# Kernel optimization log

Hardware: AMD Instinct MI355X
Metric: run time of the kernel (lower is better)

## Reference

```python
import jax, jax.numpy as jnp
import numpy as np

H = 1024  # n_hidden
T = 8192  # sequence length


def setup_inputs() -> dict:
    key = jax.random.key(0)
    ks = jax.random.split(key, 11)
    s = 1.0 / np.sqrt(H)  # torch LSTMCell/Linear default init scale
    u = lambda k, shape: jax.random.uniform(k, shape, jnp.float32, -s, s)
    return {
        "sequence": jax.random.normal(ks[0], (1, T), jnp.float32),
        # lstm1: input size 1 -> hidden H
        "w_ih1": u(ks[1], (4 * H, 1)),
        "w_hh1": u(ks[2], (4 * H, H)),
        "b_ih1": u(ks[3], (4 * H,)),
        "b_hh1": u(ks[4], (4 * H,)),
        # lstm2: hidden H -> hidden H
        "w_ih2": u(ks[5], (4 * H, H)),
        "w_hh2": u(ks[6], (4 * H, H)),
        "b_ih2": u(ks[7], (4 * H,)),
        "b_hh2": u(ks[8], (4 * H,)),
        # final linear: H -> 1
        "w_lin": u(ks[9], (1, H)),
        "b_lin": u(ks[10], (1,)),
    }


def _lstm_cell(x, h, c, w_ih, w_hh, b_ih, b_hh):
    # x: [1, in], h/c: [1, H]. PyTorch LSTMCell gate order: i, f, g, o
    gates = x @ w_ih.T + h @ w_hh.T + (b_ih + b_hh)  # [1, 4H]
    i, f, g, o = jnp.split(gates, 4, axis=-1)
    i = jax.nn.sigmoid(i)
    f = jax.nn.sigmoid(f)
    g = jnp.tanh(g)
    o = jax.nn.sigmoid(o)
    c_new = f * c + i * g
    h_new = o * jnp.tanh(c_new)
    return h_new, c_new


def reference(sequence, w_ih1, w_hh1, b_ih1, b_hh1,
              w_ih2, w_hh2, b_ih2, b_hh2, w_lin, b_lin):
    n = sequence.shape[0]  # 1
    z = jnp.zeros((n, w_hh1.shape[1]), jnp.float32)
    init = (z, z, z, z)  # h1, c1, h2, c2
    xs = sequence.T[:, :, None]  # [T, 1, 1] timesteps

    def step(carry, x_t):
        h1, c1, h2, c2 = carry
        h1, c1 = _lstm_cell(x_t, h1, c1, w_ih1, w_hh1, b_ih1, b_hh1)
        h2, c2 = _lstm_cell(h1, h2, c2, w_ih2, w_hh2, b_ih2, b_hh2)
        out = h2 @ w_lin.T + b_lin  # [1, 1]
        return (h1, c1, h2, c2), out

    _, outputs = jax.lax.scan(step, init, xs)
    return outputs  # [T, 1, 1] — stacked version of the original list of [1,1] outputs
```

## Files before the change

kernel.cpp:

```cpp
#include <hip/hip_runtime.h>

#define HID   1024
#define SEQT  8192
#define NBLK  256
#define TPB   512

#define WS_BYTES 32768

typedef float v16f __attribute__((ext_vector_type(16)));
typedef unsigned long long u64;

__device__ __forceinline__ float sig_(float x) { return 1.0f / (1.0f + expf(-x)); }

__device__ __forceinline__ u64 ldp(const u64* p) {
    return __hip_atomic_load(p, __ATOMIC_RELAXED, __HIP_MEMORY_SCOPE_AGENT);
}
__device__ __forceinline__ void stp(u64* p, u64 v) {
    __hip_atomic_store(p, v, __ATOMIC_RELAXED, __HIP_MEMORY_SCOPE_AGENT);
}

extern "C" __global__ void __launch_bounds__(TPB, 2)
lstm_hyb(const float* __restrict__ seq,
         const float* __restrict__ w_ih1, const float* __restrict__ w_hh1,
         const float* __restrict__ b_ih1, const float* __restrict__ b_hh1,
         const float* __restrict__ w_ih2, const float* __restrict__ w_hh2,
         const float* __restrict__ b_ih2, const float* __restrict__ b_hh2,
         const float* __restrict__ w_lin, const float* __restrict__ b_lin,
         float* __restrict__ out, u64* ws)
{
    __shared__ float h1s[HID];
    __shared__ float h2s[HID];
    __shared__ float seqs[SEQT];

    const int  lane = threadIdx.x & 63;
    const int  widx = threadIdx.x >> 6;
    const bool isL1 = (widx < 4);
    const int  r    = blockIdx.x * 4 + (widx & 3);

    u64* h1t = ws;
    u64* h2t = ws + 2048;

    for (int i = threadIdx.x; i < SEQT; i += TPB) seqs[i] = seq[i];

    const float* bA  = isL1 ? w_hh1 : w_ih2;
    const float* bB  = isL1 ? w_hh1 : w_hh2;
    const float* bbi = isL1 ? b_ih1 : b_ih2;
    const float* bbh = isL1 ? b_hh1 : b_hh2;
    const float  zmask = isL1 ? 0.f : 1.f;
    const float  xsel  = isL1 ? 1.f : 0.f;

    v16f A0, A1, A2, A3, B0, B1, B2, B3;
    {
        const size_t ro = (size_t)r * HID + lane;
        const float *a0 = bA + ro, *a1 = bA + (size_t)HID * HID + ro,
                    *a2 = bA + 2 * (size_t)HID * HID + ro, *a3 = bA + 3 * (size_t)HID * HID + ro;
        const float *b0 = bB + ro, *b1 = bB + (size_t)HID * HID + ro,
                    *b2 = bB + 2 * (size_t)HID * HID + ro, *b3 = bB + 3 * (size_t)HID * HID + ro;
#pragma unroll
        for (int k = 0; k < 16; ++k) {
            A0[k] = a0[64 * k]; A1[k] = a1[64 * k]; A2[k] = a2[64 * k]; A3[k] = a3[64 * k];
            B0[k] = b0[64 * k]; B1[k] = b1[64 * k]; B2[k] = b2[64 * k]; B3[k] = b3[64 * k];
        }
    }
    const float wx0 = w_ih1[0 * HID + r], wx1 = w_ih1[1 * HID + r],
                wx2 = w_ih1[2 * HID + r], wx3 = w_ih1[3 * HID + r];
    const float bb0 = bbi[0 * HID + r] + bbh[0 * HID + r];
    const float bb1 = bbi[1 * HID + r] + bbh[1 * HID + r];
    const float bb2 = bbi[2 * HID + r] + bbh[2 * HID + r];
    const float bb3 = bbi[3 * HID + r] + bbh[3 * HID + r];

    const bool carrier = (blockIdx.x == 0 && widx == 7);
    v16f WL; float blin = 0.f;
#pragma unroll
    for (int k = 0; k < 16; ++k) WL[k] = 0.f;
    if (carrier) {
#pragma unroll
        for (int k = 0; k < 16; ++k) WL[k] = w_lin[lane + 64 * k];
        blin = b_lin[0];
    }

    u64* pub = isL1 ? h1t : h2t;
    float c = 0.f;

    for (int t = 0; t <= SEQT + 1; ++t) {
        if (widx == 0 && t <= SEQT) {
            const u64* p = h1t + ((t + 1) & 1) * HID + lane;
            int guard = 0;
            for (;;) {
                int mn = 0x7fffffff;
#pragma unroll
                for (int k = 0; k < 16; ++k) {
                    u64 q = ldp(p + 64 * k);
                    h1s[lane + 64 * k] = __uint_as_float((unsigned)q);
                    mn = min(mn, (int)(q >> 32));
                }
                if (__all(mn >= t)) break;
                if (++guard > (1 << 14)) break;
            }
        }
        if (widx == 4) {
            const u64* p = h2t + (t & 1) * HID + lane;
            const int thr = t - 1;
            int guard = 0;
            for (;;) {
                int mn = 0x7fffffff;
#pragma unroll
                for (int k = 0; k < 16; ++k) {
                    u64 q = ldp(p + 64 * k);
                    h2s[lane + 64 * k] = __uint_as_float((unsigned)q);
                    mn = min(mn, (int)(q >> 32));
                }
                if (__all(mn >= thr)) break;
                if (++guard > (1 << 14)) break;
            }
        }
        __syncthreads();

        const bool act = isL1 ? (t < SEQT) : (t >= 1 && t <= SEQT);
        if (act) {
            v16f v1, v2;
#pragma unroll
            for (int k = 0; k < 16; ++k) {
                v1[k] = h1s[lane + 64 * k];
                v2[k] = h2s[lane + 64 * k] * zmask;
            }
            float a0 = 0.f, a1 = 0.f, a2 = 0.f, a3 = 0.f;
#pragma unroll
            for (int k = 0; k < 16; ++k) {
                a0 = fmaf(A0[k], v1[k], a0);
                a1 = fmaf(A1[k], v1[k], a1);
                a2 = fmaf(A2[k], v1[k], a2);
                a3 = fmaf(A3[k], v1[k], a3);
            }
#pragma unroll
            for (int k = 0; k < 16; ++k) {
                a0 = fmaf(B0[k], v2[k], a0);
                a1 = fmaf(B1[k], v2[k], a1);
                a2 = fmaf(B2[k], v2[k], a2);
                a3 = fmaf(B3[k], v2[k], a3);
            }
#pragma unroll
            for (int s = 32; s; s >>= 1) {
                a0 += __shfl_xor(a0, s);
                a1 += __shfl_xor(a1, s);
                a2 += __shfl_xor(a2, s);
                a3 += __shfl_xor(a3, s);
            }
            const float xg = xsel * ((t < SEQT) ? seqs[t] : 0.f);
            float i_ = sig_(a0 + xg * wx0 + bb0);
            float f_ = sig_(a1 + xg * wx1 + bb1);
            float g_ = tanhf(a2 + xg * wx2 + bb2);
            float o_ = sig_(a3 + xg * wx3 + bb3);
            c = f_ * c + i_ * g_;
            float h = o_ * tanhf(c);
            if (lane == 0) {
                const int ps = isL1 ? t : (t - 1);
                stp(pub + (ps & 1) * HID + r,
                    ((u64)(unsigned)(ps + 1) << 32) | (u64)__float_as_uint(h));
            }
        }

        if (carrier && t >= 2) {
            float ov = 0.f;
#pragma unroll
            for (int k = 0; k < 16; ++k) ov = fmaf(WL[k], h2s[lane + 64 * k], ov);
#pragma unroll
            for (int s = 32; s; s >>= 1) ov += __shfl_xor(ov, s);
            if (lane == 0) out[t - 2] = ov + blin;
        }

        __syncthreads();
    }
}

extern "C" void kernel_launch(void* const* d_in, const int* in_sizes, int n_in,
                              void* d_out, int out_size, void* d_ws, size_t ws_size,
                              hipStream_t stream)
{
    (void)hipMemsetAsync(d_ws, 0, WS_BYTES, stream);

    const float* seq  = (const float*)d_in[0];
    const float* wih1 = (const float*)d_in[1];
    const float* whh1 = (const float*)d_in[2];
    const float* bih1 = (const float*)d_in[3];
    const float* bhh1 = (const float*)d_in[4];
    const float* wih2 = (const float*)d_in[5];
    const float* whh2 = (const float*)d_in[6];
    const float* bih2 = (const float*)d_in[7];
    const float* bhh2 = (const float*)d_in[8];
    const float* wlin = (const float*)d_in[9];
    const float* blin = (const float*)d_in[10];
    float* out = (float*)d_out;
    u64*   ws  = (u64*)d_ws;

    hipLaunchKernelGGL(lstm_hyb, dim3(NBLK), dim3(TPB), 0, stream,
                       seq, wih1, whh1, bih1, bhh1,
                       wih2, whh2, bih2, bhh2, wlin, blin,
                       out, ws);
}
```

Baseline: 25.42 ms.

## Poll only pending h slots and pin weight registers across timesteps

The spin-wait loops now track a per-lane bitmask of slots whose producer has not yet published, and re-poll only those slots instead of reloading all 16 each iteration. Empty asm constraints pin the 128 weight floats in VGPRs so the compiler cannot spill or rematerialize them. Launch bounds drop to 1 block per CU to give the compiler more registers. The poll guard limit is lowered, and the predicated loads may add divergence overhead.

Result: slower. 56.18 ms (+121.0%).

```diff
diff --git a/kernel.cpp b/kernel.cpp
--- a/kernel.cpp
+++ b/kernel.cpp
@@ -19,7 +19,13 @@
     __hip_atomic_store(p, v, __ATOMIC_RELAXED, __HIP_MEMORY_SCOPE_AGENT);
 }
 
-extern "C" __global__ void __launch_bounds__(TPB, 2)
+#define PIN16(V)                                                               \
+    asm volatile("" : "+v"(V[0]), "+v"(V[1]), "+v"(V[2]), "+v"(V[3]),          \
+                      "+v"(V[4]), "+v"(V[5]), "+v"(V[6]), "+v"(V[7]),          \
+                      "+v"(V[8]), "+v"(V[9]), "+v"(V[10]), "+v"(V[11]),        \
+                      "+v"(V[12]), "+v"(V[13]), "+v"(V[14]), "+v"(V[15]))
+
+extern "C" __global__ void __launch_bounds__(TPB, 1)
 lstm_hyb(const float* __restrict__ seq,
          const float* __restrict__ w_ih1, const float* __restrict__ w_hh1,
          const float* __restrict__ b_ih1, const float* __restrict__ b_hh1,
@@ -62,6 +68,9 @@
             B0[k] = b0[64 * k]; B1[k] = b1[64 * k]; B2[k] = b2[64 * k]; B3[k] = b3[64 * k];
         }
     }
+    PIN16(A0); PIN16(A1); PIN16(A2); PIN16(A3);
+    PIN16(B0); PIN16(B1); PIN16(B2); PIN16(B3);
+
     const float wx0 = w_ih1[0 * HID + r], wx1 = w_ih1[1 * HID + r],
                 wx2 = w_ih1[2 * HID + r], wx3 = w_ih1[3 * HID + r];
     const float bb0 = bbi[0 * HID + r] + bbh[0 * HID + r];
@@ -83,35 +92,44 @@
     float c = 0.f;
 
     for (int t = 0; t <= SEQT + 1; ++t) {
+        PIN16(A0); PIN16(A1); PIN16(A2); PIN16(A3);
+        PIN16(B0); PIN16(B1); PIN16(B2); PIN16(B3);
+
         if (widx == 0 && t <= SEQT) {
             const u64* p = h1t + ((t + 1) & 1) * HID + lane;
+            unsigned pend = 0xFFFFu;
+            u64 q[16];
             int guard = 0;
-            for (;;) {
-                int mn = 0x7fffffff;
-#pragma unroll
-                for (int k = 0; k < 16; ++k) {
-                    u64 q = ldp(p + 64 * k);
-                    h1s[lane + 64 * k] = __uint_as_float((unsigned)q);
-                    mn = min(mn, (int)(q >> 32));
-                }
-                if (__all(mn >= t)) break;
-                if (++guard > (1 << 14)) break;
+            while (__any(pend != 0u)) {
+#pragma unroll
+                for (int k = 0; k < 16; ++k)
+                    if (pend & (1u << k)) q[k] = ldp(p + 64 * k);
+#pragma unroll
+                for (int k = 0; k < 16; ++k)
+                    if ((pend & (1u << k)) && (int)(q[k] >> 32) >= t) {
+                        h1s[lane + 64 * k] = __uint_as_float((unsigned)q[k]);
+                        pend &= ~(1u << k);
+                    }
+                if (++guard > (1 << 12)) break;
             }
         }
         if (widx == 4) {
             const u64* p = h2t + (t & 1) * HID + lane;
             const int thr = t - 1;
+            unsigned pend = 0xFFFFu;
+            u64 q[16];
             int guard = 0;
-            for (;;) {
-                int mn = 0x7fffffff;
-#pragma unroll
-                for (int k = 0; k < 16; ++k) {
-                    u64 q = ldp(p + 64 * k);
-                    h2s[lane + 64 * k] = __uint_as_float((unsigned)q);
-                    mn = min(mn, (int)(q >> 32));
-                }
-                if (__all(mn >= thr)) break;
-                if (++guard > (1 << 14)) break;
+            while (__any(pend != 0u)) {
+#pragma unroll
+                for (int k = 0; k < 16; ++k)
+                    if (pend & (1u << k)) q[k] = ldp(p + 64 * k);
+#pragma unroll
+                for (int k = 0; k < 16; ++k)
+                    if ((pend & (1u << k)) && (int)(q[k] >> 32) >= thr) {
+                        h2s[lane + 64 * k] = __uint_as_float((unsigned)q[k]);
+                        pend &= ~(1u << k);
+                    }
+                if (++guard > (1 << 12)) break;
             }
         }
         __syncthreads();
```

## Gate per-step polling on an epoch counter published by block zero

Applied to the files above, without the earlier changes.

Block zero alone polls the full tagged hidden-state buffers. Once every entry is fresh it publishes an epoch counter. The other blocks spin on that single 32-bit word before reading the 1024 tagged entries, which cuts the polling traffic on the shared buffers. The polling loads are also batched ahead of the shared-memory writes. In exchange, each step gains an extra serial hop through block zero, which may lengthen the critical path of the recurrence.

Result: slower. 32.05 ms (+26.1%).

```diff
diff --git a/kernel.cpp b/kernel.cpp
--- a/kernel.cpp
+++ b/kernel.cpp
@@ -5,10 +5,11 @@
 #define NBLK  256
 #define TPB   512
 
-#define WS_BYTES 32768
+#define WS_BYTES (32768 + 64)
 
 typedef float v16f __attribute__((ext_vector_type(16)));
 typedef unsigned long long u64;
+typedef unsigned int u32;
 
 __device__ __forceinline__ float sig_(float x) { return 1.0f / (1.0f + expf(-x)); }
 
@@ -18,15 +19,21 @@
 __device__ __forceinline__ void stp(u64* p, u64 v) {
     __hip_atomic_store(p, v, __ATOMIC_RELAXED, __HIP_MEMORY_SCOPE_AGENT);
 }
+__device__ __forceinline__ u32 ldu(const u32* p) {
+    return __hip_atomic_load(p, __ATOMIC_RELAXED, __HIP_MEMORY_SCOPE_AGENT);
+}
+__device__ __forceinline__ void stu(u32* p, u32 v) {
+    __hip_atomic_store(p, v, __ATOMIC_RELAXED, __HIP_MEMORY_SCOPE_AGENT);
+}
 
 extern "C" __global__ void __launch_bounds__(TPB, 2)
-lstm_hyb(const float* __restrict__ seq,
-         const float* __restrict__ w_ih1, const float* __restrict__ w_hh1,
-         const float* __restrict__ b_ih1, const float* __restrict__ b_hh1,
-         const float* __restrict__ w_ih2, const float* __restrict__ w_hh2,
-         const float* __restrict__ b_ih2, const float* __restrict__ b_hh2,
-         const float* __restrict__ w_lin, const float* __restrict__ b_lin,
-         float* __restrict__ out, u64* ws)
+lstm_epoch(const float* __restrict__ seq,
+           const float* __restrict__ w_ih1, const float* __restrict__ w_hh1,
+           const float* __restrict__ b_ih1, const float* __restrict__ b_hh1,
+           const float* __restrict__ w_ih2, const float* __restrict__ w_hh2,
+           const float* __restrict__ b_ih2, const float* __restrict__ b_hh2,
+           const float* __restrict__ w_lin, const float* __restrict__ b_lin,
+           float* __restrict__ out, u64* ws)
 {
     __shared__ float h1s[HID];
     __shared__ float h2s[HID];
@@ -34,11 +41,13 @@
 
     const int  lane = threadIdx.x & 63;
     const int  widx = threadIdx.x >> 6;
+    const int  blk  = blockIdx.x;
     const bool isL1 = (widx < 4);
-    const int  r    = blockIdx.x * 4 + (widx & 3);
+    const int  r    = blk * 4 + (widx & 3);
 
     u64* h1t = ws;
     u64* h2t = ws + 2048;
+    u32* ep  = (u32*)(ws + 4096);
 
     for (int i = threadIdx.x; i < SEQT; i += TPB) seqs[i] = seq[i];
 
@@ -69,7 +78,7 @@
     const float bb2 = bbi[2 * HID + r] + bbh[2 * HID + r];
     const float bb3 = bbi[3 * HID + r] + bbh[3 * HID + r];
 
-    const bool carrier = (blockIdx.x == 0 && widx == 7);
+    const bool carrier = (blk == 0 && widx == 7);
     v16f WL; float blin = 0.f;
 #pragma unroll
     for (int k = 0; k < 16; ++k) WL[k] = 0.f;
@@ -85,33 +94,83 @@
     for (int t = 0; t <= SEQT + 1; ++t) {
         if (widx == 0 && t <= SEQT) {
             const u64* p = h1t + ((t + 1) & 1) * HID + lane;
-            int guard = 0;
-            for (;;) {
-                int mn = 0x7fffffff;
-#pragma unroll
-                for (int k = 0; k < 16; ++k) {
-                    u64 q = ldp(p + 64 * k);
-                    h1s[lane + 64 * k] = __uint_as_float((unsigned)q);
-                    mn = min(mn, (int)(q >> 32));
-                }
-                if (__all(mn >= t)) break;
-                if (++guard > (1 << 14)) break;
+            if (blk == 0) {
+                int guard = 0;
+                for (;;) {
+                    int mn = 0x7fffffff;
+                    u64 q[16];
+#pragma unroll
+                    for (int k = 0; k < 16; ++k) {
+                        q[k] = ldp(p + 64 * k);
+                        mn = min(mn, (int)(q[k] >> 32));
+                    }
+#pragma unroll
+                    for (int k = 0; k < 16; ++k)
+                        h1s[lane + 64 * k] = __uint_as_float((unsigned)q[k]);
+                    if (__all(mn >= t)) break;
+                    if (++guard > (1 << 14)) break;
+                }
+                if (lane == 0) stu(ep + 0, (u32)t);
+            } else {
+                int guard = 0;
+                while ((int)ldu(ep + 0) < t)
+                    if (++guard > (1 << 15)) break;
+                int guard2 = 0;
+                for (;;) {
+                    int mn = 0x7fffffff;
+                    u64 q[16];
+#pragma unroll
+                    for (int k = 0; k < 16; ++k) {
+                        q[k] = ldp(p + 64 * k);
+                        mn = min(mn, (int)(q[k] >> 32));
+                    }
+#pragma unroll
+                    for (int k = 0; k < 16; ++k)
+                        h1s[lane + 64 * k] = __uint_as_float((unsigned)q[k]);
+                    if (__all(mn >= t)) break;
+                    if (++guard2 > (1 << 10)) break;
+                }
             }
         }
         if (widx == 4) {
             const u64* p = h2t + (t & 1) * HID + lane;
             const int thr = t - 1;
-            int guard = 0;
-            for (;;) {
-                int mn = 0x7fffffff;
-#pragma unroll
-                for (int k = 0; k < 16; ++k) {
-                    u64 q = ldp(p + 64 * k);
-                    h2s[lane + 64 * k] = __uint_as_float((unsigned)q);
-                    mn = min(mn, (int)(q >> 32));
-                }
-                if (__all(mn >= thr)) break;
-                if (++guard > (1 << 14)) break;
+            if (blk == 0) {
+                int guard = 0;
+                for (;;) {
+                    int mn = 0x7fffffff;
+                    u64 q[16];
+#pragma unroll
+                    for (int k = 0; k < 16; ++k) {
+                        q[k] = ldp(p + 64 * k);
+                        mn = min(mn, (int)(q[k] >> 32));
+                    }
+#pragma unroll
+                    for (int k = 0; k < 16; ++k)
+                        h2s[lane + 64 * k] = __uint_as_float((unsigned)q[k]);
+                    if (__all(mn >= thr)) break;
+                    if (++guard > (1 << 14)) break;
+                }
+                if (lane == 0) stu(ep + 1, (u32)t);
+            } else {
+                int guard = 0;
+                while ((int)ldu(ep + 1) < t)
+                    if (++guard > (1 << 15)) break;
+                int guard2 = 0;
+                for (;;) {
+                    int mn = 0x7fffffff;
+                    u64 q[16];
+#pragma unroll
+                    for (int k = 0; k < 16; ++k) {
+                        q[k] = ldp(p + 64 * k);
+                        mn = min(mn, (int)(q[k] >> 32));
+                    }
+#pragma unroll
+                    for (int k = 0; k < 16; ++k)
+                        h2s[lane + 64 * k] = __uint_as_float((unsigned)q[k]);
+                    if (__all(mn >= thr)) break;
+                    if (++guard2 > (1 << 10)) break;
+                }
             }
         }
         __syncthreads();
@@ -193,7 +252,7 @@
     float* out = (float*)d_out;
     u64*   ws  = (u64*)d_ws;
 
-    hipLaunchKernelGGL(lstm_hyb, dim3(NBLK), dim3(TPB), 0, stream,
+    hipLaunchKernelGGL(lstm_epoch, dim3(NBLK), dim3(TPB), 0, stream,
                        seq, wih1, whh1, bih1, bhh1,
                        wih2, whh2, bih2, bhh2, wlin, blin,
                        out, ws);
```

## Keep fp16 weight slices in LDS and use packed dot2 for gate GEMVs

Applied to the files above, without the earlier changes.

Stores each wave's weight rows as packed fp16 pairs in shared memory instead of fp32 registers, and computes the gate dot products with the fdot2 instruction on fp16 hidden-state pairs. The grid goes to 512 blocks of 256 threads, so each block handles two rows per layer. Gate nonlinearities now run only on lane 0, and the output projection reads h2 from registers. This aims to cut register pressure and the arithmetic per step on the latency-bound recurrence. The cost is fp16 rounding of weights and hidden state, which may drift over 8192 steps, plus twice as many blocks that must stay co-resident for the spin-wait scheme to work.

After: 52.86 ms. 108% more time.

```diff
diff --git a/kernel.cpp b/kernel.cpp
--- a/kernel.cpp
+++ b/kernel.cpp
@@ -2,12 +2,13 @@
 
 #define HID   1024
 #define SEQT  8192
-#define NBLK  256
-#define TPB   512
+#define NBLK  512
+#define TPB   256
 
 #define WS_BYTES 32768
 
 typedef float v16f __attribute__((ext_vector_type(16)));
+typedef _Float16 f16x2 __attribute__((ext_vector_type(2)));
 typedef unsigned long long u64;
 
 __device__ __forceinline__ float sig_(float x) { return 1.0f / (1.0f + expf(-x)); }
@@ -19,8 +20,22 @@
     __hip_atomic_store(p, v, __ATOMIC_RELAXED, __HIP_MEMORY_SCOPE_AGENT);
 }
 
+__device__ __forceinline__ f16x2 mk2(float a, float b) {
+    f16x2 v; v[0] = (_Float16)a; v[1] = (_Float16)b; return v;
+}
+
+#if __has_builtin(__builtin_amdgcn_fdot2)
+__device__ __forceinline__ float dot2(f16x2 a, f16x2 b, float c) {
+    return __builtin_amdgcn_fdot2(a, b, c, false);
+}
+#else
+__device__ __forceinline__ float dot2(f16x2 a, f16x2 b, float c) {
+    return c + (float)a[0] * (float)b[0] + (float)a[1] * (float)b[1];
+}
+#endif
+
 extern "C" __global__ void __launch_bounds__(TPB, 2)
-lstm_hyb(const float* __restrict__ seq,
+lstm_lds(const float* __restrict__ seq,
          const float* __restrict__ w_ih1, const float* __restrict__ w_hh1,
          const float* __restrict__ b_ih1, const float* __restrict__ b_hh1,
          const float* __restrict__ w_ih2, const float* __restrict__ w_hh2,
@@ -28,48 +43,53 @@
          const float* __restrict__ w_lin, const float* __restrict__ b_lin,
          float* __restrict__ out, u64* ws)
 {
-    __shared__ float h1s[HID];
-    __shared__ float h2s[HID];
-    __shared__ float seqs[SEQT];
+    __shared__ f16x2 wA[4][4][8][64];
+    __shared__ f16x2 wB[2][4][8][64];
+    __shared__ f16x2 h1p[8][64];
+    __shared__ f16x2 h2p[8][64];
 
     const int  lane = threadIdx.x & 63;
     const int  widx = threadIdx.x >> 6;
-    const bool isL1 = (widx < 4);
-    const int  r    = blockIdx.x * 4 + (widx & 3);
+    const int  blk  = blockIdx.x;
+    const bool isL1 = (widx < 2);
+    const int  r    = blk * 2 + (widx & 1);
 
     u64* h1t = ws;
     u64* h2t = ws + 2048;
 
-    for (int i = threadIdx.x; i < SEQT; i += TPB) seqs[i] = seq[i];
-
-    const float* bA  = isL1 ? w_hh1 : w_ih2;
-    const float* bB  = isL1 ? w_hh1 : w_hh2;
+    if (isL1) {
+#pragma unroll
+        for (int g = 0; g < 4; ++g) {
+            const float* row = w_hh1 + (size_t)(g * HID + r) * HID;
+#pragma unroll
+            for (int j = 0; j < 8; ++j)
+                wA[widx][g][j][lane] = mk2(row[lane + 128 * j], row[lane + 128 * j + 64]);
+        }
+    } else {
+#pragma unroll
+        for (int g = 0; g < 4; ++g) {
+            const float* ri = w_ih2 + (size_t)(g * HID + r) * HID;
+            const float* rh = w_hh2 + (size_t)(g * HID + r) * HID;
+#pragma unroll
+            for (int j = 0; j < 8; ++j) {
+                wA[widx][g][j][lane]     = mk2(ri[lane + 128 * j], ri[lane + 128 * j + 64]);
+                wB[widx - 2][g][j][lane] = mk2(rh[lane + 128 * j], rh[lane + 128 * j + 64]);
+            }
+        }
+    }
     const float* bbi = isL1 ? b_ih1 : b_ih2;
     const float* bbh = isL1 ? b_hh1 : b_hh2;
-    const float  zmask = isL1 ? 0.f : 1.f;
-    const float  xsel  = isL1 ? 1.f : 0.f;
-
-    v16f A0, A1, A2, A3, B0, B1, B2, B3;
-    {
-        const size_t ro = (size_t)r * HID + lane;
-        const float *a0 = bA + ro, *a1 = bA + (size_t)HID * HID + ro,
-                    *a2 = bA + 2 * (size_t)HID * HID + ro, *a3 = bA + 3 * (size_t)HID * HID + ro;
-        const float *b0 = bB + ro, *b1 = bB + (size_t)HID * HID + ro,
-                    *b2 = bB + 2 * (size_t)HID * HID + ro, *b3 = bB + 3 * (size_t)HID * HID + ro;
-#pragma unroll
-        for (int k = 0; k < 16; ++k) {
-            A0[k] = a0[64 * k]; A1[k] = a1[64 * k]; A2[k] = a2[64 * k]; A3[k] = a3[64 * k];
-            B0[k] = b0[64 * k]; B1[k] = b1[64 * k]; B2[k] = b2[64 * k]; B3[k] = b3[64 * k];
-        }
-    }
-    const float wx0 = w_ih1[0 * HID + r], wx1 = w_ih1[1 * HID + r],
-                wx2 = w_ih1[2 * HID + r], wx3 = w_ih1[3 * HID + r];
     const float bb0 = bbi[0 * HID + r] + bbh[0 * HID + r];
     const float bb1 = bbi[1 * HID + r] + bbh[1 * HID + r];
     const float bb2 = bbi[2 * HID + r] + bbh[2 * HID + r];
     const float bb3 = bbi[3 * HID + r] + bbh[3 * HID + r];
-
-    const bool carrier = (blockIdx.x == 0 && widx == 7);
+    float wx0 = 0.f, wx1 = 0.f, wx2 = 0.f, wx3 = 0.f;
+    if (isL1) {
+        wx0 = w_ih1[0 * HID + r]; wx1 = w_ih1[1 * HID + r];
+        wx2 = w_ih1[2 * HID + r]; wx3 = w_ih1[3 * HID + r];
+    }
+
+    const bool carrier = (blk == 0 && widx == 2);
     v16f WL; float blin = 0.f;
 #pragma unroll
     for (int k = 0; k < 16; ++k) WL[k] = 0.f;
@@ -81,63 +101,68 @@
 
     u64* pub = isL1 ? h1t : h2t;
     float c = 0.f;
+    v16f vq2;
+#pragma unroll
+    for (int k = 0; k < 16; ++k) vq2[k] = 0.f;
 
     for (int t = 0; t <= SEQT + 1; ++t) {
+        const float xt = (isL1 && t < SEQT) ? seq[t] : 0.f;
+
         if (widx == 0 && t <= SEQT) {
             const u64* p = h1t + ((t + 1) & 1) * HID + lane;
             int guard = 0;
             for (;;) {
-                int mn = 0x7fffffff;
-#pragma unroll
-                for (int k = 0; k < 16; ++k) {
-                    u64 q = ldp(p + 64 * k);
-                    h1s[lane + 64 * k] = __uint_as_float((unsigned)q);
-                    mn = min(mn, (int)(q >> 32));
-                }
+                u64 q[16]; int mn = 0x7fffffff;
+#pragma unroll
+                for (int k = 0; k < 16; ++k) { q[k] = ldp(p + 64 * k); mn = min(mn, (int)(q[k] >> 32)); }
+#pragma unroll
+                for (int j = 0; j < 8; ++j)
+                    h1p[j][lane] = mk2(__uint_as_float((unsigned)q[2 * j]),
+                                       __uint_as_float((unsigned)q[2 * j + 1]));
                 if (__all(mn >= t)) break;
-                if (++guard > (1 << 14)) break;
-            }
-        }
-        if (widx == 4) {
+                if (++guard > (1 << 13)) break;
+            }
+        }
+        if (widx == 2) {
             const u64* p = h2t + (t & 1) * HID + lane;
             const int thr = t - 1;
             int guard = 0;
             for (;;) {
-                int mn = 0x7fffffff;
-#pragma unroll
-                for (int k = 0; k < 16; ++k) {
-                    u64 q = ldp(p + 64 * k);
-                    h2s[lane + 64 * k] = __uint_as_float((unsigned)q);
-                    mn = min(mn, (int)(q >> 32));
-                }
+                u64 q[16]; int mn = 0x7fffffff;
+#pragma unroll
+                for (int k = 0; k < 16; ++k) { q[k] = ldp(p + 64 * k); mn = min(mn, (int)(q[k] >> 32)); }
+#pragma unroll
+                for (int j = 0; j < 8; ++j)
+                    h2p[j][lane] = mk2(__uint_as_float((unsigned)q[2 * j]),
+                                       __uint_as_float((unsigned)q[2 * j + 1]));
+#pragma unroll
+                for (int k = 0; k < 16; ++k) vq2[k] = __uint_as_float((unsigned)q[k]);
                 if (__all(mn >= thr)) break;
-                if (++guard > (1 << 14)) break;
+                if (++guard > (1 << 13)) break;
             }
         }
         __syncthreads();
 
         const bool act = isL1 ? (t < SEQT) : (t >= 1 && t <= SEQT);
         if (act) {
-            v16f v1, v2;
-#pragma unroll
-            for (int k = 0; k < 16; ++k) {
-                v1[k] = h1s[lane + 64 * k];
-                v2[k] = h2s[lane + 64 * k] * zmask;
-            }
             float a0 = 0.f, a1 = 0.f, a2 = 0.f, a3 = 0.f;
 #pragma unroll
-            for (int k = 0; k < 16; ++k) {
-                a0 = fmaf(A0[k], v1[k], a0);
-                a1 = fmaf(A1[k], v1[k], a1);
-                a2 = fmaf(A2[k], v1[k], a2);
-                a3 = fmaf(A3[k], v1[k], a3);
-            }
-#pragma unroll
-            for (int k = 0; k < 16; ++k) {
-                a0 = fmaf(B0[k], v2[k], a0);
-                a1 = fmaf(B1[k], v2[k], a1);
-                a2 = fmaf(B2[k], v2[k], a2);
-                a3 = fmaf(B3[k], v2[k], a3);
+            for (int j = 0; j < 8; ++j) {
+                const f16x2 h = h1p[j][lane];
+                a0 = dot2(wA[widx][0][j][lane], h, a0);
+                a1 = dot2(wA[widx][1][j][lane], h, a1);
+                a2 = dot2(wA[widx][2][j][lane], h, a2);
+                a3 = dot2(wA[widx][3][j][lane], h, a3);
+            }
+            if (!isL1) {
+#pragma unroll
+                for (int j = 0; j < 8; ++j) {
+                    const f16x2 h = h2p[j][lane];
+                    a0 = dot2(wB[widx - 2][0][j][lane], h, a0);
+                    a1 = dot2(wB[widx - 2][1][j][lane], h, a1);
+                    a2 = dot2(wB[widx - 2][2][j][lane], h, a2);
+                    a3 = dot2(wB[widx - 2][3][j][lane], h, a3);
+                }
             }
 #pragma unroll
             for (int s = 32; s; s >>= 1) {
@@ -146,14 +171,13 @@
                 a2 += __shfl_xor(a2, s);
                 a3 += __shfl_xor(a3, s);
             }
-            const float xg = xsel * ((t < SEQT) ? seqs[t] : 0.f);
-            float i_ = sig_(a0 + xg * wx0 + bb0);
-            float f_ = sig_(a1 + xg * wx1 + bb1);
-            float g_ = tanhf(a2 + xg * wx2 + bb2);
-            float o_ = sig_(a3 + xg * wx3 + bb3);
-            c = f_ * c + i_ * g_;
-            float h = o_ * tanhf(c);
             if (lane == 0) {
+                float gi = sig_(a0 + xt * wx0 + bb0);
+                float gf = sig_(a1 + xt * wx1 + bb1);
+                float gg = tanhf(a2 + xt * wx2 + bb2);
+                float go = sig_(a3 + xt * wx3 + bb3);
+                c = gf * c + gi * gg;
+                float h = go * tanhf(c);
                 const int ps = isL1 ? t : (t - 1);
                 stp(pub + (ps & 1) * HID + r,
                     ((u64)(unsigned)(ps + 1) << 32) | (u64)__float_as_uint(h));
@@ -163,7 +187,7 @@
         if (carrier && t >= 2) {
             float ov = 0.f;
 #pragma unroll
-            for (int k = 0; k < 16; ++k) ov = fmaf(WL[k], h2s[lane + 64 * k], ov);
+            for (int k = 0; k < 16; ++k) ov = fmaf(WL[k], vq2[k], ov);
 #pragma unroll
             for (int s = 32; s; s >>= 1) ov += __shfl_xor(ov, s);
             if (lane == 0) out[t - 2] = ov + blin;
@@ -193,7 +217,7 @@
     float* out = (float*)d_out;
     u64*   ws  = (u64*)d_ws;
 
-    hipLaunchKernelGGL(lstm_hyb, dim3(NBLK), dim3(TPB), 0, stream,
+    hipLaunchKernelGGL(lstm_lds, dim3(NBLK), dim3(TPB), 0, stream,
                        seq, wih1, whh1, bih1, bhh1,
                        wih2, whh2, bih2, bhh2, wlin, blin,
                        out, ws);
```
